# Optimization experiments

Measured on AMD Instinct MI355X. Metric: run time of the kernel, lower is better.

## Reference

```python
import jax, jax.numpy as jnp
import numpy as np

B, R, A, L, P = 1024, 512, 196, 2, 4  # batch, rnn_size, att_size, num_layers, num_parallels


def setup_inputs() -> dict:
    key = jax.random.key(0)
    ks = jax.random.split(key, 24)
    s = 0.02
    inp = {
        'x': jax.random.normal(ks[0], (B, R), jnp.float32),
        'att': jax.random.normal(ks[1], (B, A, R), jnp.float32),
        'inputs': jax.random.normal(ks[2], (2 * L, B, R), jnp.float32),
        # first attention block
        'Wa2a': jax.random.normal(ks[3], (A, R), jnp.float32) * s,
        'ba2a': jnp.zeros((A,), jnp.float32),
        'Wh2a': jax.random.normal(ks[4], (A, R), jnp.float32) * s,
        'bh2a': jnp.zeros((A,), jnp.float32),
        'Wd2d': jax.random.normal(ks[5], (1, A), jnp.float32) * s,
        'bd2d': jnp.zeros((1,), jnp.float32),
        # second attention block
        'Wa2a1': jax.random.normal(ks[6], (A, R), jnp.float32) * s,
        'ba2a1': jnp.zeros((A,), jnp.float32),
        'Wh2a1': jax.random.normal(ks[7], (A, R), jnp.float32) * s,
        'bh2a1': jnp.zeros((A,), jnp.float32),
        'Wd2d1': jax.random.normal(ks[8], (1, A), jnp.float32) * s,
        'bd2d1': jnp.zeros((1,), jnp.float32),
        # per-parallel LSTM gate linears, stacked over P
        'Wi2h': jax.random.normal(ks[9], (P, 4 * R, R), jnp.float32) * s,
        'bi2h': jnp.zeros((P, 4 * R), jnp.float32),
        'Wh2h': jax.random.normal(ks[10], (P, 4 * R, R), jnp.float32) * s,
        'bh2h': jnp.zeros((P, 4 * R), jnp.float32),
        'Wa2h': jax.random.normal(ks[11], (P, 4 * R, R), jnp.float32) * s,
        'ba2h': jnp.zeros((P, 4 * R), jnp.float32),
    }
    return inp


def _attend(att, h, Wa, ba, Wh, bh, Wd, bd):
    # att: [B, S, R] with S == A (code requires it); h: [B, R]
    av = jnp.einsum('bsr,ar->bsa', att, Wa) + ba            # [B, S, A]
    ah = h @ Wh.T + bh                                      # [B, A]
    # original expands h-projection along the LAST axis (unsqueeze(2).expand)
    dot = jnp.tanh(av + ah[:, :, None])                     # [B, S, A]
    score = jnp.einsum('bsa,a->bs', dot, Wd[0]) + bd[0]     # [B, S]
    w = jax.nn.softmax(score, axis=-1)
    return jnp.einsum('bsr,bs->br', att, w)                 # [B, R]


def reference(x, att, inputs, Wa2a, ba2a, Wh2a, bh2a, Wd2d, bd2d,
              Wa2a1, ba2a1, Wh2a1, bh2a1, Wd2d1, bd2d1,
              Wi2h, bi2h, Wh2h, bh2h, Wa2h, ba2h):
    R_ = x.shape[-1]
    L_ = inputs.shape[0] // 2
    outputs = []
    for i in range(L_):
        prev_c = inputs[2 * i]
        prev_h = inputs[2 * i + 1]
        xt = x if i == 0 else x + outputs[-1]
        att_res = _attend(att, prev_h, Wa2a, ba2a, Wh2a, bh2a, Wd2d, bd2d)
        # stacked per-parallel gate sums: [P, B, 4R]
        sums = (jnp.einsum('bd,pgd->pbg', xt, Wi2h) + bi2h[:, None, :]
                + jnp.einsum('bd,pgd->pbg', prev_h, Wh2h) + bh2h[:, None, :]
                + jnp.einsum('bd,pgd->pbg', att_res, Wa2h) + ba2h[:, None, :])
        ig = jax.nn.sigmoid(sums[..., :R_])
        fg = jax.nn.sigmoid(sums[..., R_:2 * R_])
        og = jax.nn.sigmoid(sums[..., 2 * R_:3 * R_])
        it = jnp.tanh(sums[..., 3 * R_:])
        nc = fg * prev_c[None] + ig * it                    # [P, B, R]
        next_c = nc.mean(axis=0)
        next_h = (og * jnp.tanh(nc)).mean(axis=0)
        att_res1 = _attend(att, next_h, Wa2a1, ba2a1, Wh2a1, bh2a1, Wd2d1, bd2d1)
        top_h = att_res1 + next_h
        outputs.append(next_c)
        outputs.append(top_h)
    return jnp.stack(outputs)  # [2L, B, R]
```

## Files before the change

kernel.cpp:

```cpp
#include <hip/hip_runtime.h>
#include <math.h>

typedef __attribute__((ext_vector_type(8))) unsigned short ushort8_t;
typedef __attribute__((ext_vector_type(8))) short bf16x8;
typedef __attribute__((ext_vector_type(4))) float f32x4;

namespace {

constexpr int Bn = 1024;
constexpr int Rn = 512;
constexpr int An = 196;
constexpr int Gn = 8192;
constexpr int Kcat = 1536;
constexpr int NP = 224;
constexpr long ROWS = (long)Bn * An;

__device__ __forceinline__ float b2f(unsigned short u) {
  union { unsigned int i; float f; } v; v.i = ((unsigned int)u) << 16; return v.f;
}
__device__ __forceinline__ unsigned short f2b(float f) {
  union { float f; unsigned int i; } v; v.f = f;
  unsigned int r = v.i + 0x7fffu + ((v.i >> 16) & 1u);
  return (unsigned short)(r >> 16);
}
__device__ __forceinline__ float sigmf(float x) {
  return __builtin_amdgcn_rcpf(1.f + __expf(-x));
}
__device__ __forceinline__ float tanhf_fast(float x) {
  const float e = __expf(2.f * x);
  return 1.f - 2.f * __builtin_amdgcn_rcpf(e + 1.f);
}

__global__ __launch_bounds__(256)
void f2b_copy(const float* __restrict__ src, unsigned short* __restrict__ dst, long n)
{
  long i = ((long)blockIdx.x * 256 + threadIdx.x) * 8;
  const long stride = (long)gridDim.x * 256 * 8;
  for (; i + 8 <= n; i += stride) {
    float4 a = *(const float4*)(src + i);
    float4 b = *(const float4*)(src + i + 4);
    ushort8_t o;
    o[0] = f2b(a.x); o[1] = f2b(a.y); o[2] = f2b(a.z); o[3] = f2b(a.w);
    o[4] = f2b(b.x); o[5] = f2b(b.y); o[6] = f2b(b.z); o[7] = f2b(b.w);
    *(ushort8_t*)(dst + i) = o;
  }
}

__global__ __launch_bounds__(256)
void pack_wpad(const float* __restrict__ Wa0, const float* __restrict__ Wa1,
               unsigned short* __restrict__ Wp)
{
  long i = ((long)blockIdx.x * 256 + threadIdx.x) * 8;
  if (i >= 2L * NP * 512) return;
  const int set = (int)(i / (NP * 512));
  const int rem = (int)(i % (NP * 512));
  const int row = rem / 512, k = rem % 512;
  ushort8_t o;
  if (row < An) {
    const float* s = (set ? Wa1 : Wa0) + (long)row * 512 + k;
    float4 a = *(const float4*)s, b = *(const float4*)(s + 4);
    o[0] = f2b(a.x); o[1] = f2b(a.y); o[2] = f2b(a.z); o[3] = f2b(a.w);
    o[4] = f2b(b.x); o[5] = f2b(b.y); o[6] = f2b(b.z); o[7] = f2b(b.w);
  } else {
    o = ushort8_t{0,0,0,0,0,0,0,0};
  }
  *(ushort8_t*)(Wp + i) = o;
}

__global__ __launch_bounds__(256)
void pack_w(const float* __restrict__ Wi, const float* __restrict__ Wh,
            const float* __restrict__ Wa, unsigned short* __restrict__ W2)
{
  long i = ((long)blockIdx.x * 256 + threadIdx.x) * 8;
  if (i >= (long)Gn * Kcat) return;
  const int g = (int)(i / Kcat);
  const int k = (int)(i % Kcat);
  const float* src = (k < 512) ? Wi + (long)g * 512 + k
                   : (k < 1024) ? Wh + (long)g * 512 + (k - 512)
                   : Wa + (long)g * 512 + (k - 1024);
  float4 a = *(const float4*)src;
  float4 b = *(const float4*)(src + 4);
  ushort8_t o;
  o[0] = f2b(a.x); o[1] = f2b(a.y); o[2] = f2b(a.z); o[3] = f2b(a.w);
  o[4] = f2b(b.x); o[5] = f2b(b.y); o[6] = f2b(b.z); o[7] = f2b(b.w);
  *(ushort8_t*)(W2 + i) = o;
}

__global__ __launch_bounds__(256)
void pack_x(const float* __restrict__ xa, const float* __restrict__ xb,
            const float* __restrict__ h, const float* __restrict__ a,
            unsigned short* __restrict__ X2)
{
  long i = ((long)blockIdx.x * 256 + threadIdx.x) * 8;
  if (i >= (long)Bn * Kcat) return;
  const int b = (int)(i / Kcat);
  const int k = (int)(i % Kcat);
  ushort8_t o;
  if (k < 512) {
    const float* s = xa + (long)b * 512 + k;
    float4 v0 = *(const float4*)s, v1 = *(const float4*)(s + 4);
    if (xb) {
      const float* s2 = xb + (long)b * 512 + k;
      float4 w0 = *(const float4*)s2, w1 = *(const float4*)(s2 + 4);
      v0.x += w0.x; v0.y += w0.y; v0.z += w0.z; v0.w += w0.w;
      v1.x += w1.x; v1.y += w1.y; v1.z += w1.z; v1.w += w1.w;
    }
    o[0] = f2b(v0.x); o[1] = f2b(v0.y); o[2] = f2b(v0.z); o[3] = f2b(v0.w);
    o[4] = f2b(v1.x); o[5] = f2b(v1.y); o[6] = f2b(v1.z); o[7] = f2b(v1.w);
  } else {
    const float* s = (k < 1024) ? h + (long)b * 512 + (k - 512)
                                : a + (long)b * 512 + (k - 1024);
    float4 v0 = *(const float4*)s, v1 = *(const float4*)(s + 4);
    o[0] = f2b(v0.x); o[1] = f2b(v0.y); o[2] = f2b(v0.z); o[3] = f2b(v0.w);
    o[4] = f2b(v1.x); o[5] = f2b(v1.y); o[6] = f2b(v1.z); o[7] = f2b(v1.w);
  }
  *(ushort8_t*)(X2 + i) = o;
}

__global__ __launch_bounds__(512)
void av_both(const unsigned short* __restrict__ A,
             const unsigned short* __restrict__ Wcat,
             const float* __restrict__ b0vec, const float* __restrict__ b1vec,
             const float* __restrict__ Wd,
             const float* __restrict__ ah0, const float* __restrict__ ah1,
             float* __restrict__ s0, float* __restrict__ s1,
             unsigned short* __restrict__ av_out)
{
  constexpr int LDP = 56;
  __shared__ unsigned short As[128 * LDP];
  __shared__ unsigned short Bs[448 * LDP];
  __shared__ float wds[NP], bas0[NP], bas1[NP];
  __shared__ float ahAs[128], ahBs[128];
  __shared__ float sbA[128], sbB[128];

  const int tid = threadIdx.x;
  const int lane = tid & 63, wid = tid >> 6;
  const int wr = wid >> 2, wc = wid & 3;
  const int fr = lane & 15, q = lane >> 4, kg = q * 8;
  const long row0 = (long)blockIdx.x * 128;

  if (tid < NP) {
    bas0[tid] = (tid < An) ? b0vec[tid] : 0.f;
    bas1[tid] = (tid < An) ? b1vec[tid] : 0.f;
    wds[tid]  = (tid < An) ? Wd[tid] : 0.f;
  }
  if (tid >= 256 && tid < 384) {
    ahAs[tid - 256] = ah0[row0 + tid - 256];
    ahBs[tid - 256] = ah1[row0 + tid - 256];
  }

  f32x4 acc[4][7] = {};

  const int arow = tid >> 2, akc = (tid & 3) * 8;
  const unsigned short* Ap = A + (row0 + arow) * 512 + akc;
  const bool bload = tid < 448;
  const unsigned short* Bp = Wcat + (long)tid * 512;

  ushort8_t pa = *(const ushort8_t*)Ap;
  ushort8_t pb0{}, pb1{}, pb2{}, pb3{};
  if (bload) {
    pb0 = *(const ushort8_t*)(Bp);
    pb1 = *(const ushort8_t*)(Bp + 8);
    pb2 = *(const ushort8_t*)(Bp + 16);
    pb3 = *(const ushort8_t*)(Bp + 24);
  }
  const int swA = arow * LDP + akc;
  const int swB = tid * LDP;

  for (int kt = 0; kt < 512; kt += 32) {
    *(ushort8_t*)&As[swA] = pa;
    if (bload) {
      *(ushort8_t*)&Bs[swB] = pb0;
      *(ushort8_t*)&Bs[swB + 8] = pb1;
      *(ushort8_t*)&Bs[swB + 16] = pb2;
      *(ushort8_t*)&Bs[swB + 24] = pb3;
    }
    if (kt + 32 < 512) {
      pa = *(const ushort8_t*)(Ap + kt + 32);
      if (bload) {
        pb0 = *(const ushort8_t*)(Bp + kt + 32);
        pb1 = *(const ushort8_t*)(Bp + kt + 40);
        pb2 = *(const ushort8_t*)(Bp + kt + 48);
        pb3 = *(const ushort8_t*)(Bp + kt + 56);
      }
    }
    __syncthreads();
    bf16x8 af[4], bfr[7];
#pragma unroll
    for (int m = 0; m < 4; ++m)
      af[m] = *(const bf16x8*)&As[(wr * 64 + m * 16 + fr) * LDP + kg];
#pragma unroll
    for (int n = 0; n < 7; ++n)
      bfr[n] = *(const bf16x8*)&Bs[(wc * 112 + n * 16 + fr) * LDP + kg];
#pragma unroll
    for (int m = 0; m < 4; ++m)
#pragma unroll
      for (int n = 0; n < 7; ++n)
        acc[m][n] = __builtin_amdgcn_mfma_f32_16x16x32_bf16(af[m], bfr[n], acc[m][n], 0, 0, 0);
    __syncthreads();
  }

  float pA[4][4], pB[4][4];
#pragma unroll
  for (int m = 0; m < 4; ++m)
#pragma unroll
    for (int j = 0; j < 4; ++j) { pA[m][j] = 0.f; pB[m][j] = 0.f; }

  if (wc < 2) {
#pragma unroll
    for (int n = 0; n < 7; ++n) {
      const int col = wc * 112 + n * 16 + fr;
      const float wd = wds[col];
      const float bv = bas0[col];
#pragma unroll
      for (int m = 0; m < 4; ++m) {
#pragma unroll
        for (int j = 0; j < 4; ++j) {
          const int rl = wr * 64 + m * 16 + q * 4 + j;
          const float av = acc[m][n][j] + bv;
          pA[m][j] += wd * tanhf_fast(av + ahAs[rl]);
          pB[m][j] += wd * tanhf_fast(av + ahBs[rl]);
        }
      }
    }
#pragma unroll
    for (int m = 0; m < 4; ++m)
#pragma unroll
      for (int j = 0; j < 4; ++j) {
#pragma unroll
        for (int off = 1; off < 16; off <<= 1) {
          pA[m][j] += __shfl_xor(pA[m][j], off);
          pB[m][j] += __shfl_xor(pB[m][j], off);
        }
      }
  } else {
#pragma unroll
    for (int n = 0; n < 7; ++n) {
      const int col1 = (wc - 2) * 112 + n * 16 + fr;
      if (col1 >= An) continue;
      const float bv = bas1[col1];
#pragma unroll
      for (int m = 0; m < 4; ++m) {
#pragma unroll
        for (int j = 0; j < 4; ++j) {
          const long row = row0 + wr * 64 + m * 16 + q * 4 + j;
          av_out[row * An + col1] = f2b(acc[m][n][j] + bv);
        }
      }
    }
  }
  __syncthreads();
  if (wc == 0 && fr == 0) {
#pragma unroll
    for (int m = 0; m < 4; ++m)
#pragma unroll
      for (int j = 0; j < 4; ++j) {
        const int rl = wr * 64 + m * 16 + q * 4 + j;
        sbA[rl] = pA[m][j]; sbB[rl] = pB[m][j];
      }
  }
  __syncthreads();
  if (wc == 1 && fr == 0) {
#pragma unroll
    for (int m = 0; m < 4; ++m)
#pragma unroll
      for (int j = 0; j < 4; ++j) {
        const int rl = wr * 64 + m * 16 + q * 4 + j;
        sbA[rl] += pA[m][j]; sbB[rl] += pB[m][j];
      }
  }
  __syncthreads();
  if (tid < 128) {
    s0[row0 + tid] = sbA[tid];
    s1[row0 + tid] = sbB[tid];
  }
}

__global__ __launch_bounds__(256)
void gemm_gate(const unsigned short* __restrict__ A, const unsigned short* __restrict__ Bm,
               const float* __restrict__ bias, float* __restrict__ C)
{
  __shared__ unsigned short As[128 * 32];
  __shared__ unsigned short Bs[128 * 32];
  const int tid = threadIdx.x;
  const int lane = tid & 63, w = tid >> 6;
  int bid = blockIdx.x;
  bid = (bid & 7) * (gridDim.x >> 3) + (bid >> 3);
  const int bx = bid & 63;
  const int by = bid >> 6;
  const long row0 = (long)by * 128;
  const long col0 = (long)bx * 128;
  const int wr = w >> 1, wc = w & 1;
  const int fr = lane & 15, q = lane >> 4;
  const int srow = lane >> 2, schk = lane & 3;

  f32x4 acc[4][4] = {};
  const unsigned short* A0 = A + row0 * Kcat + schk * 8;
  const unsigned short* B0 = Bm + col0 * Kcat + schk * 8;

  for (int kt = 0; kt < Kcat; kt += 32) {
#pragma unroll
    for (int i = 0; i < 2; ++i) {
      const int rr = (w * 2 + i) * 16 + srow;
      __builtin_amdgcn_global_load_lds(
          (const __attribute__((address_space(1))) unsigned int*)(A0 + (long)rr * Kcat + kt),
          (__attribute__((address_space(3))) unsigned int*)(As + (w * 2 + i) * 512),
          16, 0, 0);
      __builtin_amdgcn_global_load_lds(
          (const __attribute__((address_space(1))) unsigned int*)(B0 + (long)rr * Kcat + kt),
          (__attribute__((address_space(3))) unsigned int*)(Bs + (w * 2 + i) * 512),
          16, 0, 0);
    }
    __syncthreads();
    bf16x8 af[4], bfr[4];
#pragma unroll
    for (int m = 0; m < 4; ++m)
      af[m] = *(const bf16x8*)&As[(wr * 64 + m * 16 + fr) * 32 + q * 8];
#pragma unroll
    for (int n = 0; n < 4; ++n)
      bfr[n] = *(const bf16x8*)&Bs[(wc * 64 + n * 16 + fr) * 32 + q * 8];
#pragma unroll
    for (int m = 0; m < 4; ++m)
#pragma unroll
      for (int n = 0; n < 4; ++n)
        acc[m][n] = __builtin_amdgcn_mfma_f32_16x16x32_bf16(af[m], bfr[n], acc[m][n], 0, 0, 0);
    __syncthreads();
  }

  const int crow = wr * 64 + q * 4;
  const int ccol = wc * 64 + fr;
#pragma unroll
  for (int n = 0; n < 4; ++n) {
    const int col = (int)col0 + ccol + n * 16;
    const float bv = bias[col];
#pragma unroll
    for (int m = 0; m < 4; ++m) {
      const long rb = row0 + crow + m * 16;
#pragma unroll
      for (int j = 0; j < 4; ++j)
        C[(rb + j) * (long)Gn + col] = acc[m][n][j] + bv;
    }
  }
}

__global__ __launch_bounds__(256)
void gemm_bf(const unsigned short* __restrict__ A, const unsigned short* __restrict__ Bm,
             const float* __restrict__ bias, float* __restrict__ C,
             int N, int K, int ldc)
{
  constexpr int LDP = 56;
  __shared__ unsigned short As[128 * LDP];
  __shared__ unsigned short Bs[128 * LDP];
  const int tid = threadIdx.x;
  const long row0 = (long)blockIdx.y * 128;
  const int col0 = blockIdx.x * 128;
  const int wid = tid >> 6, lane = tid & 63;
  const int wr = wid >> 1, wc = wid & 1;
  const int fr = lane & 15, kg = (lane >> 4) * 8;

  f32x4 acc[4][4] = {};

  const int srow = tid >> 1;
  const int skh = tid & 1;
  const unsigned short* Ap = A + (row0 + srow) * (long)K + skh * 16;
  const int bcol = col0 + srow;
  const unsigned short* Bp = Bm + (long)(bcol < N ? bcol : N - 1) * K + skh * 16;

  ushort8_t a0 = *(const ushort8_t*)(Ap);
  ushort8_t a1 = *(const ushort8_t*)(Ap + 8);
  ushort8_t b0 = *(const ushort8_t*)(Bp);
  ushort8_t b1 = *(const ushort8_t*)(Bp + 8);

  const int sw = srow * LDP + skh * 16;
  for (int kt = 0; kt < K; kt += 32) {
    *(ushort8_t*)&As[sw] = a0;
    *(ushort8_t*)&As[sw + 8] = a1;
    *(ushort8_t*)&Bs[sw] = b0;
    *(ushort8_t*)&Bs[sw + 8] = b1;
    if (kt + 32 < K) {
      a0 = *(const ushort8_t*)(Ap + kt + 32);
      a1 = *(const ushort8_t*)(Ap + kt + 40);
      b0 = *(const ushort8_t*)(Bp + kt + 32);
      b1 = *(const ushort8_t*)(Bp + kt + 40);
    }
    __syncthreads();
    bf16x8 af[4], bfr[4];
#pragma unroll
    for (int m = 0; m < 4; ++m)
      af[m] = *(const bf16x8*)&As[(wr * 64 + m * 16 + fr) * LDP + kg];
#pragma unroll
    for (int n = 0; n < 4; ++n)
      bfr[n] = *(const bf16x8*)&Bs[(wc * 64 + n * 16 + fr) * LDP + kg];
#pragma unroll
    for (int m = 0; m < 4; ++m)
#pragma unroll
      for (int n = 0; n < 4; ++n)
        acc[m][n] = __builtin_amdgcn_mfma_f32_16x16x32_bf16(af[m], bfr[n], acc[m][n], 0, 0, 0);
    __syncthreads();
  }

  const int crow = wr * 64 + (lane >> 4) * 4;
  const int ccol = wc * 64 + fr;
#pragma unroll
  for (int n = 0; n < 4; ++n) {
    const int col = col0 + ccol + n * 16;
    if (col >= N) continue;
    const float bv = bias ? bias[col] : 0.f;
#pragma unroll
    for (int m = 0; m < 4; ++m) {
      const long rb = row0 + crow + m * 16;
#pragma unroll
      for (int j = 0; j < 4; ++j)
        C[(rb + j) * (long)ldc + col] = acc[m][n][j] + bv;
    }
  }
}

__global__ __launch_bounds__(256)
void score1(const unsigned short* __restrict__ av, const float* __restrict__ ah,
            const float* __restrict__ Wd, float* __restrict__ s0)
{
  const int row = blockIdx.x * 4 + (threadIdx.x >> 6);
  const int lane = threadIdx.x & 63;
  const unsigned short* avp = av + (long)row * An;
  const float A0 = ah[row];
  float v0 = 0.f;
  for (int a = lane; a < An; a += 64)
    v0 += Wd[a] * tanhf_fast(b2f(avp[a]) + A0);
#pragma unroll
  for (int o = 32; o; o >>= 1) v0 += __shfl_down(v0, o);
  if (lane == 0) s0[row] = v0;
}

template<bool DUAL>
__global__ __launch_bounds__(256)
void wsum2(const unsigned short* __restrict__ att,
           const float* __restrict__ w0, const float* __restrict__ w1,
           const float* __restrict__ add0,
           float* __restrict__ o0, float* __restrict__ o1)
{
  const int half = threadIdx.x >> 7;
  const int b = blockIdx.x * 2 + half;
  const int t = threadIdx.x & 127;
  const int wv = t >> 6;
  __shared__ float ws0[2][An], ws1[2][An];
  __shared__ float redm[2][2][2], redsum[2][2][2];

  const float r0a = w0[(long)b * An + t];
  const float r0b = (t + 128 < An) ? w0[(long)b * An + t + 128] : -3.0e38f;
  float r1a = -3.0e38f, r1b = -3.0e38f;
  if (DUAL) {
    r1a = w1[(long)b * An + t];
    r1b = (t + 128 < An) ? w1[(long)b * An + t + 128] : -3.0e38f;
  }
  float m0 = fmaxf(r0a, r0b), m1 = fmaxf(r1a, r1b);
#pragma unroll
  for (int o = 32; o; o >>= 1) {
    m0 = fmaxf(m0, __shfl_xor(m0, o));
    if (DUAL) m1 = fmaxf(m1, __shfl_xor(m1, o));
  }
  if ((t & 63) == 0) { redm[0][half][wv] = m0; if (DUAL) redm[1][half][wv] = m1; }
  __syncthreads();
  m0 = fmaxf(redm[0][half][0], redm[0][half][1]);
  if (DUAL) m1 = fmaxf(redm[1][half][0], redm[1][half][1]);
  const float e0a = __expf(r0a - m0);
  const float e0b = (t + 128 < An) ? __expf(r0b - m0) : 0.f;
  float sl0 = e0a + e0b, sl1 = 0.f;
  float e1a = 0.f, e1b = 0.f;
  if (DUAL) {
    e1a = __expf(r1a - m1);
    e1b = (t + 128 < An) ? __expf(r1b - m1) : 0.f;
    sl1 = e1a + e1b;
  }
#pragma unroll
  for (int o = 32; o; o >>= 1) {
    sl0 += __shfl_xor(sl0, o);
    if (DUAL) sl1 += __shfl_xor(sl1, o);
  }
  if ((t & 63) == 0) { redsum[0][half][wv] = sl0; if (DUAL) redsum[1][half][wv] = sl1; }
  __syncthreads();
  const float inv0 = __builtin_amdgcn_rcpf(redsum[0][half][0] + redsum[0][half][1]);
  ws0[half][t] = e0a * inv0;
  if (t + 128 < An) ws0[half][t + 128] = e0b * inv0;
  if (DUAL) {
    const float inv1 = __builtin_amdgcn_rcpf(redsum[1][half][0] + redsum[1][half][1]);
    ws1[half][t] = e1a * inv1;
    if (t + 128 < An) ws1[half][t + 128] = e1b * inv1;
  }
  __syncthreads();

  const unsigned short* ap = att + (long)b * An * Rn + t * 4;
  float a00 = 0, a01 = 0, a02 = 0, a03 = 0;
  float a10 = 0, a11 = 0, a12 = 0, a13 = 0;
  for (int s = 0; s < An; ++s) {
    ushort4 u = *(const ushort4*)(ap + (long)s * Rn);
    const float f0 = b2f(u.x), f1 = b2f(u.y), f2 = b2f(u.z), f3 = b2f(u.w);
    const float v0 = ws0[half][s];
    a00 = fmaf(f0, v0, a00); a01 = fmaf(f1, v0, a01);
    a02 = fmaf(f2, v0, a02); a03 = fmaf(f3, v0, a03);
    if (DUAL) {
      const float v1 = ws1[half][s];
      a10 = fmaf(f0, v1, a10); a11 = fmaf(f1, v1, a11);
      a12 = fmaf(f2, v1, a12); a13 = fmaf(f3, v1, a13);
    }
  }
  const long base = (long)b * Rn + t * 4;
  if (add0) {
    float4 ad = *(const float4*)(add0 + base);
    a00 += ad.x; a01 += ad.y; a02 += ad.z; a03 += ad.w;
  }
  *(float4*)(o0 + base) = make_float4(a00, a01, a02, a03);
  if (DUAL) *(float4*)(o1 + base) = make_float4(a10, a11, a12, a13);
}

__global__ __launch_bounds__(256)
void gates_pw(const float* __restrict__ sums, const float* __restrict__ prev_c,
              float* __restrict__ out_c, float* __restrict__ nh,
              unsigned short* __restrict__ nh_bf)
{
  const int i = blockIdx.x * 256 + threadIdx.x;
  const int b = i >> 9;
  const int r = i & 511;
  const float c = prev_c[i];
  float aC = 0.f, aH = 0.f;
#pragma unroll
  for (int p = 0; p < 4; ++p) {
    const float* sp = sums + (long)b * Gn + p * 2048 + r;
    const float ig = sigmf(sp[0]);
    const float fg = sigmf(sp[512]);
    const float og = sigmf(sp[1024]);
    const float it = tanhf_fast(sp[1536]);
    const float nc = fmaf(fg, c, ig * it);
    aC += nc;
    aH = fmaf(og, tanhf_fast(nc), aH);
  }
  out_c[i] = aC * 0.25f;
  const float hv = aH * 0.25f;
  nh[i] = hv;
  nh_bf[i] = f2b(hv);
}

__global__ __launch_bounds__(256)
void bias3(const float* __restrict__ a, const float* __restrict__ b,
           const float* __restrict__ c, float* __restrict__ o, int n)
{
  const int i = blockIdx.x * 256 + threadIdx.x;
  if (i < n) o[i] = a[i] + b[i] + c[i];
}

}

extern "C" void kernel_launch(void* const* d_in, const int* in_sizes, int n_in,
                              void* d_out, int out_size, void* d_ws, size_t ws_size,
                              hipStream_t stream)
{
  const float* x      = (const float*)d_in[0];
  const float* att    = (const float*)d_in[1];
  const float* inputs = (const float*)d_in[2];
  const float* Wa2a   = (const float*)d_in[3];
  const float* ba2a   = (const float*)d_in[4];
  const float* Wh2a   = (const float*)d_in[5];
  const float* bh2a   = (const float*)d_in[6];
  const float* Wd2d   = (const float*)d_in[7];
  const float* Wa2a1  = (const float*)d_in[9];
  const float* ba2a1  = (const float*)d_in[10];
  const float* Wh2a1  = (const float*)d_in[11];
  const float* bh2a1  = (const float*)d_in[12];
  const float* Wd2d1  = (const float*)d_in[13];
  const float* Wi2h   = (const float*)d_in[15];
  const float* bi2h   = (const float*)d_in[16];
  const float* Wh2h   = (const float*)d_in[17];
  const float* bh2h   = (const float*)d_in[18];
  const float* Wa2h   = (const float*)d_in[19];
  const float* ba2h   = (const float*)d_in[20];
  (void)in_sizes; (void)n_in; (void)out_size; (void)ws_size;

  float* out = (float*)d_out;
  const float* prev_c0 = inputs + 0 * (long)Bn * Rn;
  const float* prev_h0 = inputs + 1 * (long)Bn * Rn;
  const float* prev_c1 = inputs + 2 * (long)Bn * Rn;
  const float* prev_h1 = inputs + 3 * (long)Bn * Rn;

  char* wsp = (char*)d_ws;
  size_t off = 0;
  auto alloc = [&](size_t bytes) -> void* {
    void* p = wsp + off;
    off += (bytes + 1023) & ~(size_t)1023;
    return p;
  };
  unsigned short* att_bf  = (unsigned short*)alloc(ROWS * Rn * 2);
  unsigned short* W2      = (unsigned short*)alloc((size_t)Gn * Kcat * 2);
  unsigned short* Wpad    = (unsigned short*)alloc((size_t)2 * NP * Rn * 2);
  unsigned short* wh2a_bf = (unsigned short*)alloc((size_t)An * Rn * 2);
  unsigned short* wh2a1_bf= (unsigned short*)alloc((size_t)An * Rn * 2);
  unsigned short* h0_bf   = (unsigned short*)alloc((size_t)Bn * Rn * 2);
  unsigned short* h1_bf   = (unsigned short*)alloc((size_t)Bn * Rn * 2);
  unsigned short* nh_bf   = (unsigned short*)alloc((size_t)Bn * Rn * 2);
  unsigned short* X2      = (unsigned short*)alloc((size_t)Bn * Kcat * 2);
  unsigned short* av1_bf  = (unsigned short*)alloc(ROWS * An * 2);
  float* ahA  = (float*)alloc(ROWS * 4);
  float* ahB  = (float*)alloc(ROWS * 4);
  float* ah1  = (float*)alloc(ROWS * 4);
  float* scA  = (float*)alloc(ROWS * 4);
  float* scB  = (float*)alloc(ROWS * 4);
  float* sc1  = (float*)alloc(ROWS * 4);
  float* res0 = (float*)alloc((size_t)Bn * Rn * 4);
  float* res1 = (float*)alloc((size_t)Bn * Rn * 4);
  float* nh   = (float*)alloc((size_t)Bn * Rn * 4);
  float* bsum = (float*)alloc((size_t)Gn * 4);
  float* sums = (float*)alloc((size_t)Bn * Gn * 4);

  const dim3 blk(256);

  f2b_copy<<<dim3(50176), blk, 0, stream>>>(att, att_bf, ROWS * Rn);
  pack_wpad<<<dim3(112), blk, 0, stream>>>(Wa2a, Wa2a1, Wpad);
  f2b_copy<<<dim3(49), blk, 0, stream>>>(Wh2a,  wh2a_bf,  (long)An * Rn);
  f2b_copy<<<dim3(49), blk, 0, stream>>>(Wh2a1, wh2a1_bf, (long)An * Rn);
  f2b_copy<<<dim3(256), blk, 0, stream>>>(prev_h0, h0_bf, (long)Bn * Rn);
  f2b_copy<<<dim3(256), blk, 0, stream>>>(prev_h1, h1_bf, (long)Bn * Rn);
  pack_w<<<dim3(6144), blk, 0, stream>>>(Wi2h, Wh2h, Wa2h, W2);
  bias3<<<dim3(Gn / 256), blk, 0, stream>>>(bi2h, bh2h, ba2h, bsum, Gn);

  gemm_bf<<<dim3(2, Bn / 128), blk, 0, stream>>>(h0_bf, wh2a_bf, bh2a, ahA, An, Rn, An);
  gemm_bf<<<dim3(2, Bn / 128), blk, 0, stream>>>(h1_bf, wh2a_bf, bh2a, ahB, An, Rn, An);

  av_both<<<dim3((int)(ROWS / 128)), dim3(512), 0, stream>>>(
      att_bf, Wpad, ba2a, ba2a1, Wd2d, ahA, ahB, scA, scB, av1_bf);
  wsum2<true><<<dim3(Bn / 2), blk, 0, stream>>>(att_bf, scA, scB, (const float*)nullptr, res0, res1);

  pack_x<<<dim3(768), blk, 0, stream>>>(x, (const float*)nullptr, prev_h0, res0, X2);
  gemm_gate<<<dim3(512), blk, 0, stream>>>(X2, W2, bsum, sums);
  gates_pw<<<dim3(Bn * Rn / 256), blk, 0, stream>>>(sums, prev_c0, out + 0, nh, nh_bf);

  gemm_bf<<<dim3(2, Bn / 128), blk, 0, stream>>>(nh_bf, wh2a1_bf, bh2a1, ah1, An, Rn, An);
  score1<<<dim3((int)(ROWS / 4)), blk, 0, stream>>>(av1_bf, ah1, Wd2d1, sc1);
  wsum2<false><<<dim3(Bn / 2), blk, 0, stream>>>(att_bf, sc1, (const float*)nullptr, nh,
                                                 out + (long)Bn * Rn, (float*)nullptr);

  pack_x<<<dim3(768), blk, 0, stream>>>(x, out + (long)Bn * Rn, prev_h1, res1, X2);
  gemm_gate<<<dim3(512), blk, 0, stream>>>(X2, W2, bsum, sums);
  gates_pw<<<dim3(Bn * Rn / 256), blk, 0, stream>>>(sums, prev_c1, out + 2 * (long)Bn * Rn, nh, nh_bf);

  gemm_bf<<<dim3(2, Bn / 128), blk, 0, stream>>>(nh_bf, wh2a1_bf, bh2a1, ah1, An, Rn, An);
  score1<<<dim3((int)(ROWS / 4)), blk, 0, stream>>>(av1_bf, ah1, Wd2d1, sc1);
  wsum2<false><<<dim3(Bn / 2), blk, 0, stream>>>(att_bf, sc1, (const float*)nullptr, nh,
                                                 out + 3 * (long)Bn * Rn, (float*)nullptr);
}
```

Before: 765.7 us.

## Split attention projection kernel by weight set and load tiles directly to LDS

Replaces the combined av_both kernel, which computed both attention weight sets in one block over a 448-wide tile, with av_cs. av_cs launches a second grid dimension so each block handles one 224-wide set with smaller per-wave accumulators. Tiles move straight into shared memory through global_load_lds, replacing the register-staged prefetch, and launch bounds request higher occupancy. The two h-projection GEMMs are merged into one launch over a concatenated buffer. The trade-off is that each attention tile is now read from global memory twice, and the direct LDS loads drop the padding and the overlap of the next tile's loads with compute.

```diff
diff --git a/kernel.cpp b/kernel.cpp
--- a/kernel.cpp
+++ b/kernel.cpp
@@ -117,106 +117,98 @@
   *(ushort8_t*)(X2 + i) = o;
 }
 
-__global__ __launch_bounds__(512)
-void av_both(const unsigned short* __restrict__ A,
-             const unsigned short* __restrict__ Wcat,
-             const float* __restrict__ b0vec, const float* __restrict__ b1vec,
-             const float* __restrict__ Wd,
-             const float* __restrict__ ah0, const float* __restrict__ ah1,
-             float* __restrict__ s0, float* __restrict__ s1,
-             unsigned short* __restrict__ av_out)
-{
-  constexpr int LDP = 56;
-  __shared__ unsigned short As[128 * LDP];
-  __shared__ unsigned short Bs[448 * LDP];
-  __shared__ float wds[NP], bas0[NP], bas1[NP];
+__global__ __launch_bounds__(512, 4)
+void av_cs(const unsigned short* __restrict__ A,
+           const unsigned short* __restrict__ Wpad,
+           const float* __restrict__ b0vec, const float* __restrict__ b1vec,
+           const float* __restrict__ Wd,
+           const float* __restrict__ ah0, const float* __restrict__ ah1,
+           float* __restrict__ s0, float* __restrict__ s1,
+           unsigned short* __restrict__ av_out)
+{
+  __shared__ unsigned short As[128 * 32];
+  __shared__ unsigned short Bs[224 * 32];
+  __shared__ float wds[NP], bas[NP];
   __shared__ float ahAs[128], ahBs[128];
   __shared__ float sbA[128], sbB[128];
 
   const int tid = threadIdx.x;
-  const int lane = tid & 63, wid = tid >> 6;
-  const int wr = wid >> 2, wc = wid & 3;
-  const int fr = lane & 15, q = lane >> 4, kg = q * 8;
+  const int lane = tid & 63, w = tid >> 6;
+  const int wr = w >> 1, wc = w & 1;
+  const int fr = lane & 15, q = lane >> 4;
   const long row0 = (long)blockIdx.x * 128;
-
-  if (tid < NP) {
-    bas0[tid] = (tid < An) ? b0vec[tid] : 0.f;
-    bas1[tid] = (tid < An) ? b1vec[tid] : 0.f;
-    wds[tid]  = (tid < An) ? Wd[tid] : 0.f;
-  }
-  if (tid >= 256 && tid < 384) {
-    ahAs[tid - 256] = ah0[row0 + tid - 256];
-    ahBs[tid - 256] = ah1[row0 + tid - 256];
-  }
-
-  f32x4 acc[4][7] = {};
-
-  const int arow = tid >> 2, akc = (tid & 3) * 8;
-  const unsigned short* Ap = A + (row0 + arow) * 512 + akc;
-  const bool bload = tid < 448;
-  const unsigned short* Bp = Wcat + (long)tid * 512;
-
-  ushort8_t pa = *(const ushort8_t*)Ap;
-  ushort8_t pb0{}, pb1{}, pb2{}, pb3{};
-  if (bload) {
-    pb0 = *(const ushort8_t*)(Bp);
-    pb1 = *(const ushort8_t*)(Bp + 8);
-    pb2 = *(const ushort8_t*)(Bp + 16);
-    pb3 = *(const ushort8_t*)(Bp + 24);
-  }
-  const int swA = arow * LDP + akc;
-  const int swB = tid * LDP;
+  const int set = blockIdx.y;
+
+  if (set == 0) {
+    if (tid < NP) {
+      wds[tid] = (tid < An) ? Wd[tid] : 0.f;
+      bas[tid] = (tid < An) ? b0vec[tid] : 0.f;
+    }
+    if (tid >= 256 && tid < 384) ahAs[tid - 256] = ah0[row0 + tid - 256];
+    if (tid >= 384)              ahBs[tid - 384] = ah1[row0 + tid - 384];
+  } else {
+    if (tid < NP) bas[tid] = (tid < An) ? b1vec[tid] : 0.f;
+  }
+
+  const unsigned short* Ab = A + row0 * 512;
+  const unsigned short* Bb = Wpad + (long)set * NP * 512;
+
+  f32x4 acc[2][7] = {};
+
+  const int grow = lane >> 2;
+  const int gchk = (lane & 3) * 8;
 
   for (int kt = 0; kt < 512; kt += 32) {
-    *(ushort8_t*)&As[swA] = pa;
-    if (bload) {
-      *(ushort8_t*)&Bs[swB] = pb0;
-      *(ushort8_t*)&Bs[swB + 8] = pb1;
-      *(ushort8_t*)&Bs[swB + 16] = pb2;
-      *(ushort8_t*)&Bs[swB + 24] = pb3;
-    }
-    if (kt + 32 < 512) {
-      pa = *(const ushort8_t*)(Ap + kt + 32);
-      if (bload) {
-        pb0 = *(const ushort8_t*)(Bp + kt + 32);
-        pb1 = *(const ushort8_t*)(Bp + kt + 40);
-        pb2 = *(const ushort8_t*)(Bp + kt + 48);
-        pb3 = *(const ushort8_t*)(Bp + kt + 56);
-      }
-    }
-    __syncthreads();
-    bf16x8 af[4], bfr[7];
-#pragma unroll
-    for (int m = 0; m < 4; ++m)
-      af[m] = *(const bf16x8*)&As[(wr * 64 + m * 16 + fr) * LDP + kg];
+    {
+      const unsigned short* src = Ab + (long)(w * 16 + grow) * 512 + gchk + kt;
+      __builtin_amdgcn_global_load_lds(
+          (const __attribute__((address_space(1))) unsigned int*)src,
+          (__attribute__((address_space(3))) unsigned int*)(As + w * 512), 16, 0, 0);
+    }
+    {
+      const unsigned short* src = Bb + (long)(w * 16 + grow) * 512 + gchk + kt;
+      __builtin_amdgcn_global_load_lds(
+          (const __attribute__((address_space(1))) unsigned int*)src,
+          (__attribute__((address_space(3))) unsigned int*)(Bs + w * 512), 16, 0, 0);
+    }
+    if (w < 6) {
+      const unsigned short* src = Bb + (long)((w + 8) * 16 + grow) * 512 + gchk + kt;
+      __builtin_amdgcn_global_load_lds(
+          (const __attribute__((address_space(1))) unsigned int*)src,
+          (__attribute__((address_space(3))) unsigned int*)(Bs + (w + 8) * 512), 16, 0, 0);
+    }
+    __syncthreads();
+    bf16x8 af[2], bfr[7];
+#pragma unroll
+    for (int m = 0; m < 2; ++m)
+      af[m] = *(const bf16x8*)&As[(wr * 32 + m * 16 + fr) * 32 + q * 8];
 #pragma unroll
     for (int n = 0; n < 7; ++n)
-      bfr[n] = *(const bf16x8*)&Bs[(wc * 112 + n * 16 + fr) * LDP + kg];
-#pragma unroll
-    for (int m = 0; m < 4; ++m)
+      bfr[n] = *(const bf16x8*)&Bs[(wc * 112 + n * 16 + fr) * 32 + q * 8];
+#pragma unroll
+    for (int m = 0; m < 2; ++m)
 #pragma unroll
       for (int n = 0; n < 7; ++n)
         acc[m][n] = __builtin_amdgcn_mfma_f32_16x16x32_bf16(af[m], bfr[n], acc[m][n], 0, 0, 0);
     __syncthreads();
   }
 
-  float pA[4][4], pB[4][4];
-#pragma unroll
-  for (int m = 0; m < 4; ++m)
-#pragma unroll
-    for (int j = 0; j < 4; ++j) { pA[m][j] = 0.f; pB[m][j] = 0.f; }
-
-  if (wc < 2) {
+  if (set == 0) {
+    float pA[2][4], pB[2][4];
+#pragma unroll
+    for (int m = 0; m < 2; ++m)
+#pragma unroll
+      for (int j = 0; j < 4; ++j) { pA[m][j] = 0.f; pB[m][j] = 0.f; }
 #pragma unroll
     for (int n = 0; n < 7; ++n) {
       const int col = wc * 112 + n * 16 + fr;
       const float wd = wds[col];
-      const float bv = bas0[col];
-#pragma unroll
-      for (int m = 0; m < 4; ++m) {
+      const float bv = bas[col];
+#pragma unroll
+      for (int m = 0; m < 2; ++m) {
 #pragma unroll
         for (int j = 0; j < 4; ++j) {
-          const int rl = wr * 64 + m * 16 + q * 4 + j;
+          const int rl = wr * 32 + m * 16 + q * 4 + j;
           const float av = acc[m][n][j] + bv;
           pA[m][j] += wd * tanhf_fast(av + ahAs[rl]);
           pB[m][j] += wd * tanhf_fast(av + ahBs[rl]);
@@ -224,7 +216,7 @@
       }
     }
 #pragma unroll
-    for (int m = 0; m < 4; ++m)
+    for (int m = 0; m < 2; ++m)
 #pragma unroll
       for (int j = 0; j < 4; ++j) {
 #pragma unroll
@@ -233,46 +225,46 @@
           pB[m][j] += __shfl_xor(pB[m][j], off);
         }
       }
+    __syncthreads();
+    if (wc == 0 && fr == 0) {
+#pragma unroll
+      for (int m = 0; m < 2; ++m)
+#pragma unroll
+        for (int j = 0; j < 4; ++j) {
+          const int rl = wr * 32 + m * 16 + q * 4 + j;
+          sbA[rl] = pA[m][j]; sbB[rl] = pB[m][j];
+        }
+    }
+    __syncthreads();
+    if (wc == 1 && fr == 0) {
+#pragma unroll
+      for (int m = 0; m < 2; ++m)
+#pragma unroll
+        for (int j = 0; j < 4; ++j) {
+          const int rl = wr * 32 + m * 16 + q * 4 + j;
+          sbA[rl] += pA[m][j]; sbB[rl] += pB[m][j];
+        }
+    }
+    __syncthreads();
+    if (tid < 128) {
+      s0[row0 + tid] = sbA[tid];
+      s1[row0 + tid] = sbB[tid];
+    }
   } else {
 #pragma unroll
     for (int n = 0; n < 7; ++n) {
-      const int col1 = (wc - 2) * 112 + n * 16 + fr;
-      if (col1 >= An) continue;
-      const float bv = bas1[col1];
-#pragma unroll
-      for (int m = 0; m < 4; ++m) {
+      const int col = wc * 112 + n * 16 + fr;
+      if (col >= An) continue;
+      const float bv = bas[col];
+#pragma unroll
+      for (int m = 0; m < 2; ++m) {
 #pragma unroll
         for (int j = 0; j < 4; ++j) {
-          const long row = row0 + wr * 64 + m * 16 + q * 4 + j;
-          av_out[row * An + col1] = f2b(acc[m][n][j] + bv);
+          const long row = row0 + wr * 32 + m * 16 + q * 4 + j;
+          av_out[row * An + col] = f2b(acc[m][n][j] + bv);
         }
       }
     }
-  }
-  __syncthreads();
-  if (wc == 0 && fr == 0) {
-#pragma unroll
-    for (int m = 0; m < 4; ++m)
-#pragma unroll
-      for (int j = 0; j < 4; ++j) {
-        const int rl = wr * 64 + m * 16 + q * 4 + j;
-        sbA[rl] = pA[m][j]; sbB[rl] = pB[m][j];
-      }
-  }
-  __syncthreads();
-  if (wc == 1 && fr == 0) {
-#pragma unroll
-    for (int m = 0; m < 4; ++m)
-#pragma unroll
-      for (int j = 0; j < 4; ++j) {
-        const int rl = wr * 64 + m * 16 + q * 4 + j;
-        sbA[rl] += pA[m][j]; sbB[rl] += pB[m][j];
-      }
-  }
-  __syncthreads();
-  if (tid < 128) {
-    s0[row0 + tid] = sbA[tid];
-    s1[row0 + tid] = sbB[tid];
   }
 }
 
@@ -593,13 +585,11 @@
   unsigned short* Wpad    = (unsigned short*)alloc((size_t)2 * NP * Rn * 2);
   unsigned short* wh2a_bf = (unsigned short*)alloc((size_t)An * Rn * 2);
   unsigned short* wh2a1_bf= (unsigned short*)alloc((size_t)An * Rn * 2);
-  unsigned short* h0_bf   = (unsigned short*)alloc((size_t)Bn * Rn * 2);
-  unsigned short* h1_bf   = (unsigned short*)alloc((size_t)Bn * Rn * 2);
+  unsigned short* h01_bf  = (unsigned short*)alloc((size_t)2 * Bn * Rn * 2);
   unsigned short* nh_bf   = (unsigned short*)alloc((size_t)Bn * Rn * 2);
   unsigned short* X2      = (unsigned short*)alloc((size_t)Bn * Kcat * 2);
   unsigned short* av1_bf  = (unsigned short*)alloc(ROWS * An * 2);
-  float* ahA  = (float*)alloc(ROWS * 4);
-  float* ahB  = (float*)alloc(ROWS * 4);
+  float* ahAB = (float*)alloc((size_t)2 * ROWS * 4);
   float* ah1  = (float*)alloc(ROWS * 4);
   float* scA  = (float*)alloc(ROWS * 4);
   float* scB  = (float*)alloc(ROWS * 4);
@@ -610,21 +600,23 @@
   float* bsum = (float*)alloc((size_t)Gn * 4);
   float* sums = (float*)alloc((size_t)Bn * Gn * 4);
 
+  float* ahA = ahAB;
+  float* ahB = ahAB + ROWS;
+
   const dim3 blk(256);
 
   f2b_copy<<<dim3(50176), blk, 0, stream>>>(att, att_bf, ROWS * Rn);
   pack_wpad<<<dim3(112), blk, 0, stream>>>(Wa2a, Wa2a1, Wpad);
   f2b_copy<<<dim3(49), blk, 0, stream>>>(Wh2a,  wh2a_bf,  (long)An * Rn);
   f2b_copy<<<dim3(49), blk, 0, stream>>>(Wh2a1, wh2a1_bf, (long)An * Rn);
-  f2b_copy<<<dim3(256), blk, 0, stream>>>(prev_h0, h0_bf, (long)Bn * Rn);
-  f2b_copy<<<dim3(256), blk, 0, stream>>>(prev_h1, h1_bf, (long)Bn * Rn);
+  f2b_copy<<<dim3(256), blk, 0, stream>>>(prev_h0, h01_bf, (long)Bn * Rn);
+  f2b_copy<<<dim3(256), blk, 0, stream>>>(prev_h1, h01_bf + (long)Bn * Rn, (long)Bn * Rn);
   pack_w<<<dim3(6144), blk, 0, stream>>>(Wi2h, Wh2h, Wa2h, W2);
   bias3<<<dim3(Gn / 256), blk, 0, stream>>>(bi2h, bh2h, ba2h, bsum, Gn);
 
-  gemm_bf<<<dim3(2, Bn / 128), blk, 0, stream>>>(h0_bf, wh2a_bf, bh2a, ahA, An, Rn, An);
-  gemm_bf<<<dim3(2, Bn / 128), blk, 0, stream>>>(h1_bf, wh2a_bf, bh2a, ahB, An, Rn, An);
-
-  av_both<<<dim3((int)(ROWS / 128)), dim3(512), 0, stream>>>(
+  gemm_bf<<<dim3(2, 16), blk, 0, stream>>>(h01_bf, wh2a_bf, bh2a, ahA, An, Rn, An);
+
+  av_cs<<<dim3((int)(ROWS / 128), 2), dim3(512), 0, stream>>>(
       att_bf, Wpad, ba2a, ba2a1, Wd2d, ahA, ahB, scA, scB, av1_bf);
   wsum2<true><<<dim3(Bn / 2), blk, 0, stream>>>(att_bf, scA, scB, (const float*)nullptr, res0, res1);
 
```

Result: faster. 714.5 us (-6.7%).
